# Performance work log

Measured on AMD Instinct MI355X. Metric: run time of the kernel, lower is better.

Reference implementation:

```python
import jax, jax.numpy as jnp
import numpy as np

EPS_PRE = 1e-05   # added to raw scores, matches `+ 1e-05`
EPS_NORM = 1e-12  # torch F.normalize default eps


def setup_inputs() -> dict:
    key = jax.random.key(0)
    k1, k2, k3, k4 = jax.random.split(key, 4)
    B, H, S, D = 2, 16, 2048, 64
    query = jax.random.normal(k1, (B, H, S, D), dtype=jnp.float32)
    keys = jax.random.normal(k2, (B, H, S, D), dtype=jnp.float32)
    vals = jax.random.normal(k3, (B, H, S, D), dtype=jnp.float32)
    mask = jax.random.randint(k4, (B, 1, S, S), 0, 2, dtype=jnp.int32)
    return {"query": query, "keys": keys, "vals": vals, "mask": mask}


def reference(query, keys, vals, mask):
    # [B,H,S,S] raw scores; +1e-5 matches the torch module
    preattn = jnp.einsum("bhqd,bhkd->bhqk", query, keys) + EPS_PRE
    preattn = jnp.where(mask == 0, jnp.zeros((), preattn.dtype), preattn)
    # F.normalize: x / max(||x||_2, eps) along last dim
    norm = jnp.sqrt(jnp.sum(preattn * preattn, axis=-1, keepdims=True))
    attn = preattn / jnp.maximum(norm, EPS_NORM)
    # dropout is identity in eval mode
    return jnp.einsum("bhqk,bhkd->bhqd", attn, vals)
```

## Files before the change

### kernel.cpp

```cpp
#include <hip/hip_runtime.h>


constexpr int Sdim = 2048;
constexpr int Ddim = 64;
constexpr int BQ = 64;
constexpr int BK = 64;
constexpr int LD = 72;

typedef __attribute__((ext_vector_type(8))) short short8;
typedef __attribute__((ext_vector_type(4))) float f32x4;

#define MFMA(acc, a, b) (acc) = __builtin_amdgcn_mfma_f32_16x16x32_bf16((a), (b), (acc), 0, 0, 0)

__device__ __forceinline__ unsigned bf_hi(float x) {
    union { float f; unsigned u; } v; v.f = x;
    return (v.u + 0x7fffu + ((v.u >> 16) & 1u)) >> 16;
}
__device__ __forceinline__ float bf_f(unsigned h) {
    union { unsigned u; float f; } v; v.u = h << 16; return v.f;
}

__global__ __launch_bounds__(256, 2) void lka_mfma(
    const float* __restrict__ Q, const float* __restrict__ K,
    const float* __restrict__ V, const int* __restrict__ M,
    float* __restrict__ O)
{
    __shared__ unsigned short Qh[BQ * LD], Ql[BQ * LD];
    __shared__ unsigned short Kh[BK * LD], Kl[BK * LD];
    __shared__ unsigned short Vh[Ddim * LD];
    __shared__ unsigned short Ph[BQ * LD];
    __shared__ float ssq_tab[4][BQ];

    const int tid  = threadIdx.x;
    const int w    = tid >> 6;
    const int lane = tid & 63;
    const int l15  = lane & 15;
    const int g    = lane >> 4;
    const int bh   = blockIdx.y;
    const int b    = bh >> 4;
    const int q0   = blockIdx.x * BQ;

    const float* Qp = Q + (size_t)bh * Sdim * Ddim;
    const float* Kp = K + (size_t)bh * Sdim * Ddim;
    const float* Vp = V + (size_t)bh * Sdim * Ddim;
    const int*   Mp = M + (size_t)b * Sdim * Sdim;
    float*       Op = O + (size_t)bh * Sdim * Ddim;

#pragma unroll
    for (int it = 0; it < 4; ++it) {
        int idx = tid + it * 256;
        int row = idx >> 4, c4 = idx & 15;
        float4 v = *(const float4*)(Qp + (size_t)(q0 + row) * Ddim + c4 * 4);
        unsigned h0 = bf_hi(v.x), h1 = bf_hi(v.y), h2 = bf_hi(v.z), h3 = bf_hi(v.w);
        *(uint2*)(&Qh[row * LD + c4 * 4]) = make_uint2(h0 | (h1 << 16), h2 | (h3 << 16));
        *(uint2*)(&Ql[row * LD + c4 * 4]) = make_uint2(
            bf_hi(v.x - bf_f(h0)) | (bf_hi(v.y - bf_f(h1)) << 16),
            bf_hi(v.z - bf_f(h2)) | (bf_hi(v.w - bf_f(h3)) << 16));
    }
    __syncthreads();

#define QFRAG(t)                                                               \
    short8 qb##t##h0, qb##t##h1, qb##t##l0, qb##t##l1;                         \
    {                                                                          \
        const int brow = 16 * (t) + l15;                                       \
        qb##t##h0 = *(const short8*)(&Qh[brow * LD + g * 8]);                  \
        qb##t##h1 = *(const short8*)(&Qh[brow * LD + 32 + g * 8]);             \
        qb##t##l0 = *(const short8*)(&Ql[brow * LD + g * 8]);                  \
        qb##t##l1 = *(const short8*)(&Ql[brow * LD + 32 + g * 8]);             \
    }
    QFRAG(0) QFRAG(1) QFRAG(2) QFRAG(3)
#undef QFRAG

    f32x4 acc0 = {0.f,0.f,0.f,0.f}, acc1 = {0.f,0.f,0.f,0.f};
    f32x4 acc2 = {0.f,0.f,0.f,0.f}, acc3 = {0.f,0.f,0.f,0.f};
    float ssq0 = 0.f, ssq1 = 0.f, ssq2 = 0.f, ssq3 = 0.f;

    for (int k0 = 0; k0 < Sdim; k0 += BK) {
        __syncthreads();

#pragma unroll
        for (int it = 0; it < 4; ++it) {
            int idx = tid + it * 256;
            int row = idx >> 4, c4 = idx & 15;
            {
                float4 v = *(const float4*)(Kp + (size_t)(k0 + row) * Ddim + c4 * 4);
                unsigned h0 = bf_hi(v.x), h1 = bf_hi(v.y), h2 = bf_hi(v.z), h3 = bf_hi(v.w);
                *(uint2*)(&Kh[row * LD + c4 * 4]) = make_uint2(h0 | (h1 << 16), h2 | (h3 << 16));
                *(uint2*)(&Kl[row * LD + c4 * 4]) = make_uint2(
                    bf_hi(v.x - bf_f(h0)) | (bf_hi(v.y - bf_f(h1)) << 16),
                    bf_hi(v.z - bf_f(h2)) | (bf_hi(v.w - bf_f(h3)) << 16));
            }
            {
                float4 v = *(const float4*)(Vp + (size_t)(k0 + row) * Ddim + c4 * 4);
                int kb = row >> 3, ko = row & 7;
#define VSTORE(i, comp)                                                        \
                {                                                              \
                    int d = c4 * 4 + (i);                                      \
                    int off = d * LD + (((kb ^ (d >> 3)) << 3) | ko);          \
                    Vh[off] = (unsigned short)bf_hi(v.comp);                   \
                }
                VSTORE(0, x) VSTORE(1, y) VSTORE(2, z) VSTORE(3, w)
#undef VSTORE
            }
        }
        __syncthreads();

        const int arow = 16 * w + l15;
        short8 aKh0 = *(const short8*)(&Kh[arow * LD + g * 8]);
        short8 aKh1 = *(const short8*)(&Kh[arow * LD + 32 + g * 8]);
        short8 aKl0 = *(const short8*)(&Kl[arow * LD + g * 8]);
        short8 aKl1 = *(const short8*)(&Kl[arow * LD + 32 + g * 8]);

#define QKT_TILE(t, sacc)                                                      \
        f32x4 sacc = {0.f, 0.f, 0.f, 0.f};                                     \
        {                                                                      \
            MFMA(sacc, aKh0, qb##t##h0); MFMA(sacc, aKh1, qb##t##h1);          \
            MFMA(sacc, aKh0, qb##t##l0); MFMA(sacc, aKh1, qb##t##l1);          \
            MFMA(sacc, aKl0, qb##t##h0); MFMA(sacc, aKl1, qb##t##h1);          \
        }
        QKT_TILE(0, s0) QKT_TILE(1, s1) QKT_TILE(2, s2) QKT_TILE(3, s3)
#undef QKT_TILE

        const int kcol = k0 + 16 * w + 4 * g;
#define PARK(t, sacc, ssq)                                                     \
        {                                                                      \
            const int qrow = q0 + 16 * (t) + l15;                              \
            int4 mm = *(const int4*)(Mp + (size_t)qrow * Sdim + kcol);         \
            float x0 = mm.x ? sacc.x + 1e-5f : 0.f;                            \
            float x1 = mm.y ? sacc.y + 1e-5f : 0.f;                            \
            float x2 = mm.z ? sacc.z + 1e-5f : 0.f;                            \
            float x3 = mm.w ? sacc.w + 1e-5f : 0.f;                            \
            ssq += x0 * x0 + x1 * x1 + x2 * x2 + x3 * x3;                      \
            int po = (16 * (t) + l15) * LD + 16 * w + 4 * g;                   \
            *(uint2*)(&Ph[po]) = make_uint2(bf_hi(x0) | (bf_hi(x1) << 16),     \
                                            bf_hi(x2) | (bf_hi(x3) << 16));   \
        }
        PARK(0, s0, ssq0) PARK(1, s1, ssq1) PARK(2, s2, ssq2) PARK(3, s3, ssq3)
#undef PARK
        __syncthreads();

        const int prow = 16 * w + l15;
        short8 aPh0 = *(const short8*)(&Ph[prow * LD + g * 8]);
        short8 aPh1 = *(const short8*)(&Ph[prow * LD + 32 + g * 8]);

#define PV_TILE(t, acc)                                                        \
        {                                                                      \
            const int drow = 16 * (t) + l15;                                   \
            const int sw = drow >> 3;                                          \
            short8 vb0 = *(const short8*)(&Vh[drow * LD + (((0 + g) ^ sw) << 3)]); \
            short8 vb1 = *(const short8*)(&Vh[drow * LD + (((4 + g) ^ sw) << 3)]); \
            MFMA(acc, aPh0, vb0); MFMA(acc, aPh1, vb1);                        \
        }
        PV_TILE(0, acc0) PV_TILE(1, acc1) PV_TILE(2, acc2) PV_TILE(3, acc3)
#undef PV_TILE
    }

    ssq0 += __shfl_xor(ssq0, 16, 64); ssq0 += __shfl_xor(ssq0, 32, 64);
    ssq1 += __shfl_xor(ssq1, 16, 64); ssq1 += __shfl_xor(ssq1, 32, 64);
    ssq2 += __shfl_xor(ssq2, 16, 64); ssq2 += __shfl_xor(ssq2, 32, 64);
    ssq3 += __shfl_xor(ssq3, 16, 64); ssq3 += __shfl_xor(ssq3, 32, 64);
    if (lane < 16) {
        ssq_tab[w][l15]      = ssq0;
        ssq_tab[w][16 + l15] = ssq1;
        ssq_tab[w][32 + l15] = ssq2;
        ssq_tab[w][48 + l15] = ssq3;
    }
    __syncthreads();

#define OUTR(reg, comp)                                                        \
    {                                                                          \
        const int q = 16 * w + 4 * g + (reg);                                  \
        float sum = ssq_tab[0][q] + ssq_tab[1][q] + ssq_tab[2][q] + ssq_tab[3][q]; \
        float rn = 1.0f / fmaxf(sqrtf(sum), 1e-12f);                           \
        float* orow = Op + (size_t)(q0 + q) * Ddim + l15;                      \
        orow[0]  = acc0.comp * rn;                                             \
        orow[16] = acc1.comp * rn;                                             \
        orow[32] = acc2.comp * rn;                                             \
        orow[48] = acc3.comp * rn;                                             \
    }
    OUTR(0, x) OUTR(1, y) OUTR(2, z) OUTR(3, w)
#undef OUTR
}

extern "C" void kernel_launch(void* const* d_in, const int* in_sizes, int n_in,
                              void* d_out, int out_size, void* d_ws, size_t ws_size,
                              hipStream_t stream) {
    const float* Q = (const float*)d_in[0];
    const float* K = (const float*)d_in[1];
    const float* V = (const float*)d_in[2];
    const int*   M = (const int*)d_in[3];
    float*       O = (float*)d_out;

    const int BH = in_sizes[0] / (Sdim * Ddim);
    dim3 grid(Sdim / BQ, BH);
    lka_mfma<<<grid, dim3(256), 0, stream>>>(Q, K, V, M, O);
}
```

Baseline: 266.5 us.

## Double-buffer K/V tiles with register prefetch and hoist mask loads

K and V shared tiles are double-buffered. The next tile's global loads are issued into registers at the top of each iteration and written to the alternate buffer after the score stage, so global latency overlaps the MFMA work. Mask loads are hoisted to the start of the iteration, and Q staging reuses the second K buffer to limit LDS growth. The cost is more registers, which may reduce occupancy under launch_bounds(256,2), and the syncs per iteration are rearranged.

Result: no change. 268.5 us (+0.8%).

```diff
diff --git a/kernel.cpp b/kernel.cpp
--- a/kernel.cpp
+++ b/kernel.cpp
@@ -25,9 +25,8 @@
     const float* __restrict__ V, const int* __restrict__ M,
     float* __restrict__ O)
 {
-    __shared__ unsigned short Qh[BQ * LD], Ql[BQ * LD];
-    __shared__ unsigned short Kh[BK * LD], Kl[BK * LD];
-    __shared__ unsigned short Vh[Ddim * LD];
+    __shared__ unsigned short Kh[2][BK * LD], Kl[2][BK * LD];
+    __shared__ unsigned short Vh[2][Ddim * LD];
     __shared__ unsigned short Ph[BQ * LD];
     __shared__ float ssq_tab[4][BQ];
 
@@ -36,6 +35,8 @@
     const int lane = tid & 63;
     const int l15  = lane & 15;
     const int g    = lane >> 4;
+    const int r0   = tid >> 4;
+    const int c4   = tid & 15;
     const int bh   = blockIdx.y;
     const int b    = bh >> 4;
     const int q0   = blockIdx.x * BQ;
@@ -46,16 +47,34 @@
     const int*   Mp = M + (size_t)b * Sdim * Sdim;
     float*       Op = O + (size_t)bh * Sdim * Ddim;
 
+#define KSTAGE_W(dstH, dstL, row, vreg)                                        \
+    {                                                                          \
+        unsigned h0 = bf_hi(vreg.x), h1 = bf_hi(vreg.y),                       \
+                 h2 = bf_hi(vreg.z), h3 = bf_hi(vreg.w);                       \
+        *(uint2*)(&dstH[(row) * LD + c4 * 4]) =                                \
+            make_uint2(h0 | (h1 << 16), h2 | (h3 << 16));                      \
+        *(uint2*)(&dstL[(row) * LD + c4 * 4]) = make_uint2(                    \
+            bf_hi(vreg.x - bf_f(h0)) | (bf_hi(vreg.y - bf_f(h1)) << 16),       \
+            bf_hi(vreg.z - bf_f(h2)) | (bf_hi(vreg.w - bf_f(h3)) << 16));      \
+    }
+#define VSTAGE_W(dstV, row, vreg)                                              \
+    {                                                                          \
+        int kb = (row) >> 3, ko = (row) & 7;                                   \
+        { int d = c4 * 4 + 0; dstV[d * LD + (((kb ^ (d >> 3)) << 3) | ko)] = (unsigned short)bf_hi(vreg.x); } \
+        { int d = c4 * 4 + 1; dstV[d * LD + (((kb ^ (d >> 3)) << 3) | ko)] = (unsigned short)bf_hi(vreg.y); } \
+        { int d = c4 * 4 + 2; dstV[d * LD + (((kb ^ (d >> 3)) << 3) | ko)] = (unsigned short)bf_hi(vreg.z); } \
+        { int d = c4 * 4 + 3; dstV[d * LD + (((kb ^ (d >> 3)) << 3) | ko)] = (unsigned short)bf_hi(vreg.w); } \
+    }
+
 #pragma unroll
     for (int it = 0; it < 4; ++it) {
-        int idx = tid + it * 256;
-        int row = idx >> 4, c4 = idx & 15;
-        float4 v = *(const float4*)(Qp + (size_t)(q0 + row) * Ddim + c4 * 4);
-        unsigned h0 = bf_hi(v.x), h1 = bf_hi(v.y), h2 = bf_hi(v.z), h3 = bf_hi(v.w);
-        *(uint2*)(&Qh[row * LD + c4 * 4]) = make_uint2(h0 | (h1 << 16), h2 | (h3 << 16));
-        *(uint2*)(&Ql[row * LD + c4 * 4]) = make_uint2(
-            bf_hi(v.x - bf_f(h0)) | (bf_hi(v.y - bf_f(h1)) << 16),
-            bf_hi(v.z - bf_f(h2)) | (bf_hi(v.w - bf_f(h3)) << 16));
+        const int row = r0 + 16 * it;
+        float4 qv = *(const float4*)(Qp + (size_t)(q0 + row) * Ddim + c4 * 4);
+        KSTAGE_W(Kh[1], Kl[1], row, qv);
+        float4 kv = *(const float4*)(Kp + (size_t)row * Ddim + c4 * 4);
+        KSTAGE_W(Kh[0], Kl[0], row, kv);
+        float4 vv = *(const float4*)(Vp + (size_t)row * Ddim + c4 * 4);
+        VSTAGE_W(Vh[0], row, vv);
     }
     __syncthreads();
 
@@ -63,53 +82,50 @@
     short8 qb##t##h0, qb##t##h1, qb##t##l0, qb##t##l1;                         \
     {                                                                          \
         const int brow = 16 * (t) + l15;                                       \
-        qb##t##h0 = *(const short8*)(&Qh[brow * LD + g * 8]);                  \
-        qb##t##h1 = *(const short8*)(&Qh[brow * LD + 32 + g * 8]);             \
-        qb##t##l0 = *(const short8*)(&Ql[brow * LD + g * 8]);                  \
-        qb##t##l1 = *(const short8*)(&Ql[brow * LD + 32 + g * 8]);             \
+        qb##t##h0 = *(const short8*)(&Kh[1][brow * LD + g * 8]);               \
+        qb##t##h1 = *(const short8*)(&Kh[1][brow * LD + 32 + g * 8]);          \
+        qb##t##l0 = *(const short8*)(&Kl[1][brow * LD + g * 8]);               \
+        qb##t##l1 = *(const short8*)(&Kl[1][brow * LD + 32 + g * 8]);          \
     }
     QFRAG(0) QFRAG(1) QFRAG(2) QFRAG(3)
 #undef QFRAG
+    __syncthreads();
 
     f32x4 acc0 = {0.f,0.f,0.f,0.f}, acc1 = {0.f,0.f,0.f,0.f};
     f32x4 acc2 = {0.f,0.f,0.f,0.f}, acc3 = {0.f,0.f,0.f,0.f};
     float ssq0 = 0.f, ssq1 = 0.f, ssq2 = 0.f, ssq3 = 0.f;
 
-    for (int k0 = 0; k0 < Sdim; k0 += BK) {
-        __syncthreads();
-
-#pragma unroll
-        for (int it = 0; it < 4; ++it) {
-            int idx = tid + it * 256;
-            int row = idx >> 4, c4 = idx & 15;
-            {
-                float4 v = *(const float4*)(Kp + (size_t)(k0 + row) * Ddim + c4 * 4);
-                unsigned h0 = bf_hi(v.x), h1 = bf_hi(v.y), h2 = bf_hi(v.z), h3 = bf_hi(v.w);
-                *(uint2*)(&Kh[row * LD + c4 * 4]) = make_uint2(h0 | (h1 << 16), h2 | (h3 << 16));
-                *(uint2*)(&Kl[row * LD + c4 * 4]) = make_uint2(
-                    bf_hi(v.x - bf_f(h0)) | (bf_hi(v.y - bf_f(h1)) << 16),
-                    bf_hi(v.z - bf_f(h2)) | (bf_hi(v.w - bf_f(h3)) << 16));
-            }
-            {
-                float4 v = *(const float4*)(Vp + (size_t)(k0 + row) * Ddim + c4 * 4);
-                int kb = row >> 3, ko = row & 7;
-#define VSTORE(i, comp)                                                        \
-                {                                                              \
-                    int d = c4 * 4 + (i);                                      \
-                    int off = d * LD + (((kb ^ (d >> 3)) << 3) | ko);          \
-                    Vh[off] = (unsigned short)bf_hi(v.comp);                   \
-                }
-                VSTORE(0, x) VSTORE(1, y) VSTORE(2, z) VSTORE(3, w)
-#undef VSTORE
-            }
-        }
-        __syncthreads();
-
+    int cur = 0;
+    for (int k0 = 0; k0 < Sdim; k0 += BK, cur ^= 1) {
+        const bool hasn = (k0 + BK) < Sdim;
+        const int  k0n  = k0 + BK;
+
+        float4 kp0, kp1, kp2, kp3, vp0, vp1, vp2, vp3;
+        if (hasn) {
+            const float* KpN = Kp + (size_t)k0n * Ddim;
+            const float* VpN = Vp + (size_t)k0n * Ddim;
+            kp0 = *(const float4*)(KpN + (size_t)(r0     ) * Ddim + c4 * 4);
+            kp1 = *(const float4*)(KpN + (size_t)(r0 + 16) * Ddim + c4 * 4);
+            kp2 = *(const float4*)(KpN + (size_t)(r0 + 32) * Ddim + c4 * 4);
+            kp3 = *(const float4*)(KpN + (size_t)(r0 + 48) * Ddim + c4 * 4);
+            vp0 = *(const float4*)(VpN + (size_t)(r0     ) * Ddim + c4 * 4);
+            vp1 = *(const float4*)(VpN + (size_t)(r0 + 16) * Ddim + c4 * 4);
+            vp2 = *(const float4*)(VpN + (size_t)(r0 + 32) * Ddim + c4 * 4);
+            vp3 = *(const float4*)(VpN + (size_t)(r0 + 48) * Ddim + c4 * 4);
+        }
+        const int kcol = k0 + 16 * w + 4 * g;
+        const int4 mm0 = *(const int4*)(Mp + (size_t)(q0      + l15) * Sdim + kcol);
+        const int4 mm1 = *(const int4*)(Mp + (size_t)(q0 + 16 + l15) * Sdim + kcol);
+        const int4 mm2 = *(const int4*)(Mp + (size_t)(q0 + 32 + l15) * Sdim + kcol);
+        const int4 mm3 = *(const int4*)(Mp + (size_t)(q0 + 48 + l15) * Sdim + kcol);
+
+        const unsigned short* KhC = Kh[cur];
+        const unsigned short* KlC = Kl[cur];
         const int arow = 16 * w + l15;
-        short8 aKh0 = *(const short8*)(&Kh[arow * LD + g * 8]);
-        short8 aKh1 = *(const short8*)(&Kh[arow * LD + 32 + g * 8]);
-        short8 aKl0 = *(const short8*)(&Kl[arow * LD + g * 8]);
-        short8 aKl1 = *(const short8*)(&Kl[arow * LD + 32 + g * 8]);
+        short8 aKh0 = *(const short8*)(&KhC[arow * LD + g * 8]);
+        short8 aKh1 = *(const short8*)(&KhC[arow * LD + 32 + g * 8]);
+        short8 aKl0 = *(const short8*)(&KlC[arow * LD + g * 8]);
+        short8 aKl1 = *(const short8*)(&KlC[arow * LD + 32 + g * 8]);
 
 #define QKT_TILE(t, sacc)                                                      \
         f32x4 sacc = {0.f, 0.f, 0.f, 0.f};                                     \
@@ -121,15 +137,12 @@
         QKT_TILE(0, s0) QKT_TILE(1, s1) QKT_TILE(2, s2) QKT_TILE(3, s3)
 #undef QKT_TILE
 
-        const int kcol = k0 + 16 * w + 4 * g;
 #define PARK(t, sacc, ssq)                                                     \
         {                                                                      \
-            const int qrow = q0 + 16 * (t) + l15;                              \
-            int4 mm = *(const int4*)(Mp + (size_t)qrow * Sdim + kcol);         \
-            float x0 = mm.x ? sacc.x + 1e-5f : 0.f;                            \
-            float x1 = mm.y ? sacc.y + 1e-5f : 0.f;                            \
-            float x2 = mm.z ? sacc.z + 1e-5f : 0.f;                            \
-            float x3 = mm.w ? sacc.w + 1e-5f : 0.f;                            \
+            float x0 = mm##t.x ? sacc.x + 1e-5f : 0.f;                         \
+            float x1 = mm##t.y ? sacc.y + 1e-5f : 0.f;                         \
+            float x2 = mm##t.z ? sacc.z + 1e-5f : 0.f;                         \
+            float x3 = mm##t.w ? sacc.w + 1e-5f : 0.f;                         \
             ssq += x0 * x0 + x1 * x1 + x2 * x2 + x3 * x3;                      \
             int po = (16 * (t) + l15) * LD + 16 * w + 4 * g;                   \
             *(uint2*)(&Ph[po]) = make_uint2(bf_hi(x0) | (bf_hi(x1) << 16),     \
@@ -137,8 +150,23 @@
         }
         PARK(0, s0, ssq0) PARK(1, s1, ssq1) PARK(2, s2, ssq2) PARK(3, s3, ssq3)
 #undef PARK
+
+        if (hasn) {
+            unsigned short* KhN = Kh[cur ^ 1];
+            unsigned short* KlN = Kl[cur ^ 1];
+            unsigned short* VhN = Vh[cur ^ 1];
+            KSTAGE_W(KhN, KlN, r0,      kp0);
+            KSTAGE_W(KhN, KlN, r0 + 16, kp1);
+            KSTAGE_W(KhN, KlN, r0 + 32, kp2);
+            KSTAGE_W(KhN, KlN, r0 + 48, kp3);
+            VSTAGE_W(VhN, r0,      vp0);
+            VSTAGE_W(VhN, r0 + 16, vp1);
+            VSTAGE_W(VhN, r0 + 32, vp2);
+            VSTAGE_W(VhN, r0 + 48, vp3);
+        }
         __syncthreads();
 
+        const unsigned short* VhC = Vh[cur];
         const int prow = 16 * w + l15;
         short8 aPh0 = *(const short8*)(&Ph[prow * LD + g * 8]);
         short8 aPh1 = *(const short8*)(&Ph[prow * LD + 32 + g * 8]);
@@ -147,12 +175,13 @@
         {                                                                      \
             const int drow = 16 * (t) + l15;                                   \
             const int sw = drow >> 3;                                          \
-            short8 vb0 = *(const short8*)(&Vh[drow * LD + (((0 + g) ^ sw) << 3)]); \
-            short8 vb1 = *(const short8*)(&Vh[drow * LD + (((4 + g) ^ sw) << 3)]); \
+            short8 vb0 = *(const short8*)(&VhC[drow * LD + (((0 + g) ^ sw) << 3)]); \
+            short8 vb1 = *(const short8*)(&VhC[drow * LD + (((4 + g) ^ sw) << 3)]); \
             MFMA(acc, aPh0, vb0); MFMA(acc, aPh1, vb1);                        \
         }
         PV_TILE(0, acc0) PV_TILE(1, acc1) PV_TILE(2, acc2) PV_TILE(3, acc3)
 #undef PV_TILE
+        __syncthreads();
     }
 
     ssq0 += __shfl_xor(ssq0, 16, 64); ssq0 += __shfl_xor(ssq0, 32, 64);
```
